# Optimization experiments

Hardware: AMD Instinct MI355X
Metric: run time of the kernel (lower is better)

Reference implementation:

```python
import jax, jax.numpy as jnp
import numpy as np

B, H, S, D = 2, 16, 4096, 64
WIN = 512
HALF = WIN // 2  # stride of the sliding window


def setup_inputs() -> dict:
    key = jax.random.key(0)
    kq, kk, kv = jax.random.split(key, 3)
    Q = jax.random.normal(kq, (B, H, S, D), dtype=jnp.float32)
    K = jax.random.normal(kk, (B, H, S, D), dtype=jnp.float32)
    V = jax.random.normal(kv, (B, H, S, D), dtype=jnp.float32)
    scale = jnp.float32(1.0 / np.sqrt(D))
    return {"Q": Q, "K": K, "V": V, "scale": scale}


def _window_attn(Q, K, V, scale):
    # sigmoid attention normalized to sum 1 over keys (use_sigmoid=True path)
    scores = jnp.einsum('...qd,...kd->...qk', Q, K) * scale
    attn = jax.nn.sigmoid(scores)
    attn = attn / jnp.sum(attn, axis=-1, keepdims=True)
    return jnp.einsum('...qk,...kd->...qd', attn, V)


def reference(Q, K, V, scale):
    b, h, s, d = Q.shape
    n_full = (s - WIN) // HALF + 1
    starts = jnp.arange(n_full) * HALF
    idx = starts[:, None] + jnp.arange(WIN)
    Qw = Q[:, :, idx, :]
    Kw = K[:, :, idx, :]
    Vw = V[:, :, idx, :]
    out_w = _window_attn(Qw, Kw, Vw, scale)

    # trailing partial window of length HALF starting at n_full*HALF
    p0 = n_full * HALF
    out_p = _window_attn(Q[:, :, p0:, :], K[:, :, p0:, :], V[:, :, p0:, :], scale)  # [b,h,HALF,d]

    alpha = jnp.linspace(0.0, 1.0, HALF, dtype=Q.dtype).reshape(1, 1, HALF, 1)
    fh = out_w[:, :, :, :HALF, :]   # first halves of each full window
    sh = out_w[:, :, :, HALF:, :]   # second halves

    a5 = alpha[:, :, None]          # [1,1,1,HALF,1]
    # overlap blend: region starting at w*HALF (w>=1) mixes window w-1's 2nd half
    # with window w's 1st half
    mid = (1 - a5) * sh[:, :, :-1] + a5 * fh[:, :, 1:]     # [b,h,n_full-1,HALF,d]
    mid = mid.reshape(b, h, (n_full - 1) * HALF, d)
    tail = (1 - alpha) * sh[:, :, -1] + alpha * out_p       # [b,h,HALF,d]
    return jnp.concatenate([fh[:, :, 0], mid, tail], axis=2)
```

## Files before the change

kernel.cpp:

```cpp
#include <hip/hip_runtime.h>
#include <stdint.h>

#define NB 2
#define NH 16
#define SEQ 4096
#define DD 64
#define NM 16
#define QB 256
#define CH 256
#define VSTR 528

typedef __attribute__((ext_vector_type(8)))  __bf16 bf16x8;
typedef __attribute__((ext_vector_type(16))) float  f32x16;
typedef __attribute__((ext_vector_type(2)))  unsigned int u32x2;

static __device__ __forceinline__ f32x16 zero16() {
    f32x16 z;
#pragma unroll
    for (int i = 0; i < 16; i++) z[i] = 0.0f;
    return z;
}

__global__ void __launch_bounds__(512, 2)
swa_kernel(const float* __restrict__ Q, const float* __restrict__ K,
           const float* __restrict__ V, const float* __restrict__ scale_p,
           float* __restrict__ out)
{
    int lid = (int)blockIdx.x;
    lid = (lid & 7) * 64 + (lid >> 3);
    const int m  = lid & 15;
    const int bh = lid >> 4;

    const float scale = scale_p[0];
    const float* Qb = Q + (size_t)bh * SEQ * DD;
    const float* Kb = K + (size_t)bh * SEQ * DD;
    const float* Vb = V + (size_t)bh * SEQ * DD;
    float*       Ob = out + (size_t)bh * SEQ * DD;

    const int tid  = threadIdx.x;
    const int lane = tid & 63;
    const int w    = tid >> 6;
    const int l31  = lane & 31;
    const int h5   = lane >> 5;

    __shared__ __align__(16) unsigned char vt[64 * VSTR];

    bf16x8 qf[4];
    {
        const float* qp = Qb + (size_t)(m * QB + w * 32 + l31) * DD + 8 * h5;
#pragma unroll
        for (int s = 0; s < 4; s++) {
            float4 a = *(const float4*)(qp + 16 * s);
            float4 b = *(const float4*)(qp + 16 * s + 4);
            bf16x8 f;
            f[0] = (__bf16)a.x; f[1] = (__bf16)a.y; f[2] = (__bf16)a.z; f[3] = (__bf16)a.w;
            f[4] = (__bf16)b.x; f[5] = (__bf16)b.y; f[6] = (__bf16)b.z; f[7] = (__bf16)b.w;
            qf[s] = f;
        }
    }

    f32x16 accA0 = zero16(), accA1 = zero16();
    f32x16 accB0 = zero16(), accB1 = zero16();
    float dA = 0.0f, dB = 0.0f;

    for (int ci = 0; ci < 3; ci++) {
        const int ck = (m - 1 + ci) * CH;
        if (ck < 0 || ck >= SEQ) continue;
        const bool inA = (m > 0) && (ci <= 1);
        const bool inB = (ci >= 1);

        __syncthreads();
        {
            const int kk = (tid & 127) * 2;
            const int dg = tid >> 7;
            const float* vp0 = Vb + (size_t)(ck + kk) * DD + dg * 16;
            const float* vp1 = vp0 + DD;
#pragma unroll
            for (int j = 0; j < 16; j += 4) {
                float4 a = *(const float4*)(vp0 + j);
                float4 b = *(const float4*)(vp1 + j);
                float av[4] = {a.x, a.y, a.z, a.w};
                float bv[4] = {b.x, b.y, b.z, b.w};
#pragma unroll
                for (int e = 0; e < 4; e++) {
                    union { __bf16 h[2]; uint32_t u; } pk;
                    pk.h[0] = (__bf16)av[e];
                    pk.h[1] = (__bf16)bv[e];
                    *(uint32_t*)(vt + (size_t)(dg * 16 + j + e) * VSTR + kk * 2) = pk.u;
                }
            }
        }
        __syncthreads();

        for (int kt = 0; kt < 8; kt++) {
            const float* kp = Kb + (size_t)(ck + kt * 32 + l31) * DD + 8 * h5;
            f32x16 st = zero16();
#pragma unroll
            for (int s = 0; s < 4; s++) {
                float4 a = *(const float4*)(kp + 16 * s);
                float4 b = *(const float4*)(kp + 16 * s + 4);
                bf16x8 f;
                f[0] = (__bf16)a.x; f[1] = (__bf16)a.y; f[2] = (__bf16)a.z; f[3] = (__bf16)a.w;
                f[4] = (__bf16)b.x; f[5] = (__bf16)b.y; f[6] = (__bf16)b.z; f[7] = (__bf16)b.w;
                st = __builtin_amdgcn_mfma_f32_32x32x16_bf16(f, qf[s], st, 0, 0, 0);
            }

            uint32_t wv[8];
            float dsum = 0.0f;
#pragma unroll
            for (int i = 0; i < 8; i++) {
                float e0 = __expf(-st[2 * i] * scale);
                float e1 = __expf(-st[2 * i + 1] * scale);
                float p0 = __builtin_amdgcn_rcpf(1.0f + e0);
                float p1 = __builtin_amdgcn_rcpf(1.0f + e1);
                union { __bf16 h[2]; uint32_t u; } pk;
                pk.h[0] = (__bf16)p0;
                pk.h[1] = (__bf16)p1;
                wv[i] = pk.u;
                dsum += (float)pk.h[0] + (float)pk.h[1];
            }
            if (inA) dA += dsum;
            if (inB) dB += dsum;

            u32x2 rA = __builtin_amdgcn_permlane32_swap(wv[0], wv[2], false, false);
            u32x2 rB = __builtin_amdgcn_permlane32_swap(wv[1], wv[3], false, false);
            u32x2 rC = __builtin_amdgcn_permlane32_swap(wv[4], wv[6], false, false);
            u32x2 rD = __builtin_amdgcn_permlane32_swap(wv[5], wv[7], false, false);
            union { uint32_t u[4]; bf16x8 v; } A0, A1;
            A0.u[0] = rA[0]; A0.u[1] = rB[0]; A0.u[2] = rA[1]; A0.u[3] = rB[1];
            A1.u[0] = rC[0]; A1.u[1] = rD[0]; A1.u[2] = rC[1]; A1.u[3] = rD[1];

            const unsigned char* vrow0 = vt + (size_t)l31 * VSTR;
            const unsigned char* vrow1 = vt + (size_t)(32 + l31) * VSTR;
            const int ko = kt * 64 + h5 * 16;
            bf16x8 v00 = *(const bf16x8*)(vrow0 + ko);
            bf16x8 v01 = *(const bf16x8*)(vrow0 + ko + 32);
            bf16x8 v10 = *(const bf16x8*)(vrow1 + ko);
            bf16x8 v11 = *(const bf16x8*)(vrow1 + ko + 32);

            if (inA) {
                accA0 = __builtin_amdgcn_mfma_f32_32x32x16_bf16(A0.v, v00, accA0, 0, 0, 0);
                accA0 = __builtin_amdgcn_mfma_f32_32x32x16_bf16(A1.v, v01, accA0, 0, 0, 0);
                accA1 = __builtin_amdgcn_mfma_f32_32x32x16_bf16(A0.v, v10, accA1, 0, 0, 0);
                accA1 = __builtin_amdgcn_mfma_f32_32x32x16_bf16(A1.v, v11, accA1, 0, 0, 0);
            }
            if (inB) {
                accB0 = __builtin_amdgcn_mfma_f32_32x32x16_bf16(A0.v, v00, accB0, 0, 0, 0);
                accB0 = __builtin_amdgcn_mfma_f32_32x32x16_bf16(A1.v, v01, accB0, 0, 0, 0);
                accB1 = __builtin_amdgcn_mfma_f32_32x32x16_bf16(A0.v, v10, accB1, 0, 0, 0);
                accB1 = __builtin_amdgcn_mfma_f32_32x32x16_bf16(A1.v, v11, accB1, 0, 0, 0);
            }
        }
    }

    const float dAt = dA + __shfl_xor(dA, 32, 64);
    const float dBt = dB + __shfl_xor(dB, 32, 64);
    const float invA = __builtin_amdgcn_rcpf(dAt);
    const float invB = __builtin_amdgcn_rcpf(dBt);

#pragma unroll
    for (int r = 0; r < 16; r++) {
        const int cr = (r & 3) + 8 * (r >> 2) + 4 * h5;
        const int j  = w * 32 + cr;
        const float ia = __shfl(invA, cr, 64);
        const float ib = __shfl(invB, cr, 64);
        float o0, o1;
        if (m == 0) {
            o0 = accB0[r] * ib;
            o1 = accB1[r] * ib;
        } else {
            const float alpha = (float)j * (1.0f / 255.0f);
            const float a0 = accA0[r] * ia, b0 = accB0[r] * ib;
            const float a1 = accA1[r] * ia, b1 = accB1[r] * ib;
            o0 = (1.0f - alpha) * a0 + alpha * b0;
            o1 = (1.0f - alpha) * a1 + alpha * b1;
        }
        float* orow = Ob + (size_t)(m * QB + j) * DD;
        orow[l31]      = o0;
        orow[32 + l31] = o1;
    }
}

extern "C" void kernel_launch(void* const* d_in, const int* in_sizes, int n_in,
                              void* d_out, int out_size, void* d_ws, size_t ws_size,
                              hipStream_t stream) {
    const float* Q = (const float*)d_in[0];
    const float* K = (const float*)d_in[1];
    const float* V = (const float*)d_in[2];
    const float* s = (const float*)d_in[3];
    float* out = (float*)d_out;
    dim3 grid(NB * NH * NM, 1, 1);
    dim3 block(512, 1, 1);
    hipLaunchKernelGGL(swa_kernel, grid, block, 0, stream, Q, K, V, s, out);
}
```

Measured before the change: 226.2 us.

## Stage K in LDS as bf16, XOR-swizzle V layout, fold scale into Q

K chunks are now loaded cooperatively once per 256-key chunk, converted to bf16 and stored in LDS in MFMA-fragment order. Each wave reads its K operands from LDS instead of re-reading fp32 K from global memory and converting it per tile. The V transpose buffer drops its padded stride for an XOR-swizzled layout to avoid bank conflicts. The scale is folded into Q before the bf16 conversion, which removes a multiply per score, and the denominator now sums fp32 sigmoids instead of the bf16-rounded values. The launch-bounds occupancy hint is raised from 2 to 4, but LDS use doubles to 64 KB per block, which may limit how many blocks fit on a CU.

```diff
diff --git a/kernel.cpp b/kernel.cpp
--- a/kernel.cpp
+++ b/kernel.cpp
@@ -8,7 +8,6 @@
 #define NM 16
 #define QB 256
 #define CH 256
-#define VSTR 528
 
 typedef __attribute__((ext_vector_type(8)))  __bf16 bf16x8;
 typedef __attribute__((ext_vector_type(16))) float  f32x16;
@@ -21,7 +20,7 @@
     return z;
 }
 
-__global__ void __launch_bounds__(512, 2)
+__global__ void __launch_bounds__(512, 4)
 swa_kernel(const float* __restrict__ Q, const float* __restrict__ K,
            const float* __restrict__ V, const float* __restrict__ scale_p,
            float* __restrict__ out)
@@ -43,7 +42,8 @@
     const int l31  = lane & 31;
     const int h5   = lane >> 5;
 
-    __shared__ __align__(16) unsigned char vt[64 * VSTR];
+    __shared__ __align__(16) unsigned char kl[32768];
+    __shared__ __align__(16) unsigned char vl[32768];
 
     bf16x8 qf[4];
     {
@@ -53,8 +53,10 @@
             float4 a = *(const float4*)(qp + 16 * s);
             float4 b = *(const float4*)(qp + 16 * s + 4);
             bf16x8 f;
-            f[0] = (__bf16)a.x; f[1] = (__bf16)a.y; f[2] = (__bf16)a.z; f[3] = (__bf16)a.w;
-            f[4] = (__bf16)b.x; f[5] = (__bf16)b.y; f[6] = (__bf16)b.z; f[7] = (__bf16)b.w;
+            f[0] = (__bf16)(a.x * scale); f[1] = (__bf16)(a.y * scale);
+            f[2] = (__bf16)(a.z * scale); f[3] = (__bf16)(a.w * scale);
+            f[4] = (__bf16)(b.x * scale); f[5] = (__bf16)(b.y * scale);
+            f[6] = (__bf16)(b.z * scale); f[7] = (__bf16)(b.w * scale);
             qf[s] = f;
         }
     }
@@ -71,6 +73,25 @@
 
         __syncthreads();
         {
+            const int key = tid >> 1, half = tid & 1;
+            const float* kp = Kb + (size_t)(ck + key) * DD + 32 * half;
+            float fl[32];
+#pragma unroll
+            for (int i = 0; i < 8; i++) {
+                float4 t = *(const float4*)(kp + 4 * i);
+                fl[4 * i] = t.x; fl[4 * i + 1] = t.y; fl[4 * i + 2] = t.z; fl[4 * i + 3] = t.w;
+            }
+#pragma unroll
+            for (int g = 0; g < 4; g++) {
+                const int sp = g >> 1, hg = g & 1;
+                const int s = 2 * half + sp;
+                bf16x8 o;
+#pragma unroll
+                for (int e = 0; e < 8; e++) o[e] = (__bf16)fl[16 * sp + 8 * hg + e];
+                *(bf16x8*)(kl + ((key >> 5) * 4 + s) * 1024 + ((key & 31) + 32 * hg) * 16) = o;
+            }
+        }
+        {
             const int kk = (tid & 127) * 2;
             const int dg = tid >> 7;
             const float* vp0 = Vb + (size_t)(ck + kk) * DD + dg * 16;
@@ -86,38 +107,33 @@
                     union { __bf16 h[2]; uint32_t u; } pk;
                     pk.h[0] = (__bf16)av[e];
                     pk.h[1] = (__bf16)bv[e];
-                    *(uint32_t*)(vt + (size_t)(dg * 16 + j + e) * VSTR + kk * 2) = pk.u;
+                    const int row = dg * 16 + j + e;
+                    *(uint32_t*)(vl + ((row * 512 + kk * 2) ^ ((row & 15) << 4))) = pk.u;
                 }
             }
         }
         __syncthreads();
 
         for (int kt = 0; kt < 8; kt++) {
-            const float* kp = Kb + (size_t)(ck + kt * 32 + l31) * DD + 8 * h5;
+            const unsigned char* kfb = kl + kt * 4096 + lane * 16;
             f32x16 st = zero16();
 #pragma unroll
             for (int s = 0; s < 4; s++) {
-                float4 a = *(const float4*)(kp + 16 * s);
-                float4 b = *(const float4*)(kp + 16 * s + 4);
-                bf16x8 f;
-                f[0] = (__bf16)a.x; f[1] = (__bf16)a.y; f[2] = (__bf16)a.z; f[3] = (__bf16)a.w;
-                f[4] = (__bf16)b.x; f[5] = (__bf16)b.y; f[6] = (__bf16)b.z; f[7] = (__bf16)b.w;
-                st = __builtin_amdgcn_mfma_f32_32x32x16_bf16(f, qf[s], st, 0, 0, 0);
+                bf16x8 kf = *(const bf16x8*)(kfb + s * 1024);
+                st = __builtin_amdgcn_mfma_f32_32x32x16_bf16(kf, qf[s], st, 0, 0, 0);
             }
 
             uint32_t wv[8];
             float dsum = 0.0f;
 #pragma unroll
             for (int i = 0; i < 8; i++) {
-                float e0 = __expf(-st[2 * i] * scale);
-                float e1 = __expf(-st[2 * i + 1] * scale);
-                float p0 = __builtin_amdgcn_rcpf(1.0f + e0);
-                float p1 = __builtin_amdgcn_rcpf(1.0f + e1);
+                float p0 = __builtin_amdgcn_rcpf(1.0f + __expf(-st[2 * i]));
+                float p1 = __builtin_amdgcn_rcpf(1.0f + __expf(-st[2 * i + 1]));
+                dsum += p0 + p1;
                 union { __bf16 h[2]; uint32_t u; } pk;
                 pk.h[0] = (__bf16)p0;
                 pk.h[1] = (__bf16)p1;
                 wv[i] = pk.u;
-                dsum += (float)pk.h[0] + (float)pk.h[1];
             }
             if (inA) dA += dsum;
             if (inB) dB += dsum;
@@ -130,13 +146,12 @@
             A0.u[0] = rA[0]; A0.u[1] = rB[0]; A0.u[2] = rA[1]; A0.u[3] = rB[1];
             A1.u[0] = rC[0]; A1.u[1] = rD[0]; A1.u[2] = rC[1]; A1.u[3] = rD[1];
 
-            const unsigned char* vrow0 = vt + (size_t)l31 * VSTR;
-            const unsigned char* vrow1 = vt + (size_t)(32 + l31) * VSTR;
             const int ko = kt * 64 + h5 * 16;
-            bf16x8 v00 = *(const bf16x8*)(vrow0 + ko);
-            bf16x8 v01 = *(const bf16x8*)(vrow0 + ko + 32);
-            bf16x8 v10 = *(const bf16x8*)(vrow1 + ko);
-            bf16x8 v11 = *(const bf16x8*)(vrow1 + ko + 32);
+            const int x0 = (l31 & 15) << 4;
+            bf16x8 v00 = *(const bf16x8*)(vl + ((l31 * 512 + ko) ^ x0));
+            bf16x8 v01 = *(const bf16x8*)(vl + ((l31 * 512 + ko + 32) ^ x0));
+            bf16x8 v10 = *(const bf16x8*)(vl + (((32 + l31) * 512 + ko) ^ x0));
+            bf16x8 v11 = *(const bf16x8*)(vl + (((32 + l31) * 512 + ko + 32) ^ x0));
 
             if (inA) {
                 accA0 = __builtin_amdgcn_mfma_f32_32x32x16_bf16(A0.v, v00, accA0, 0, 0, 0);
```

Result: slower. 389.2 us (+72.1%).

## Pre-convert K to bf16 in a workspace pass and prefetch K tiles

Applied to the files above, without the earlier changes.

Adds a separate pass that converts K from fp32 to bf16 into the workspace. The attention kernel then reads the bf16 K with register double-buffered prefetch of the next tile, which halves K read traffic and removes the conversion that was repeated inside the inner loop. The scale is also folded into Q when it is loaded, and the denominator is summed from fp32 probabilities instead of rounded ones. This costs an extra kernel launch plus a full K read and write, and the fast path only runs if the workspace is large enough.

```diff
diff --git a/kernel.cpp b/kernel.cpp
--- a/kernel.cpp
+++ b/kernel.cpp
@@ -21,10 +21,29 @@
     return z;
 }
 
+__global__ void __launch_bounds__(256)
+cvt_k_kernel(const float* __restrict__ K, __bf16* __restrict__ kw)
+{
+    const size_t gid = (size_t)blockIdx.x * 256 + threadIdx.x;
+    const float* src = K + gid * 16;
+    float4 a = *(const float4*)(src);
+    float4 b = *(const float4*)(src + 4);
+    float4 c = *(const float4*)(src + 8);
+    float4 d = *(const float4*)(src + 12);
+    bf16x8 o0, o1;
+    o0[0] = (__bf16)a.x; o0[1] = (__bf16)a.y; o0[2] = (__bf16)a.z; o0[3] = (__bf16)a.w;
+    o0[4] = (__bf16)b.x; o0[5] = (__bf16)b.y; o0[6] = (__bf16)b.z; o0[7] = (__bf16)b.w;
+    o1[0] = (__bf16)c.x; o1[1] = (__bf16)c.y; o1[2] = (__bf16)c.z; o1[3] = (__bf16)c.w;
+    o1[4] = (__bf16)d.x; o1[5] = (__bf16)d.y; o1[6] = (__bf16)d.z; o1[7] = (__bf16)d.w;
+    *(bf16x8*)(kw + gid * 16)     = o0;
+    *(bf16x8*)(kw + gid * 16 + 8) = o1;
+}
+
+template<bool PRE>
 __global__ void __launch_bounds__(512, 2)
 swa_kernel(const float* __restrict__ Q, const float* __restrict__ K,
            const float* __restrict__ V, const float* __restrict__ scale_p,
-           float* __restrict__ out)
+           const __bf16* __restrict__ kw, float* __restrict__ out)
 {
     int lid = (int)blockIdx.x;
     lid = (lid & 7) * 64 + (lid >> 3);
@@ -35,6 +54,7 @@
     const float* Qb = Q + (size_t)bh * SEQ * DD;
     const float* Kb = K + (size_t)bh * SEQ * DD;
     const float* Vb = V + (size_t)bh * SEQ * DD;
+    const __bf16* kwb = kw + (size_t)bh * SEQ * DD;
     float*       Ob = out + (size_t)bh * SEQ * DD;
 
     const int tid  = threadIdx.x;
@@ -53,8 +73,10 @@
             float4 a = *(const float4*)(qp + 16 * s);
             float4 b = *(const float4*)(qp + 16 * s + 4);
             bf16x8 f;
-            f[0] = (__bf16)a.x; f[1] = (__bf16)a.y; f[2] = (__bf16)a.z; f[3] = (__bf16)a.w;
-            f[4] = (__bf16)b.x; f[5] = (__bf16)b.y; f[6] = (__bf16)b.z; f[7] = (__bf16)b.w;
+            f[0] = (__bf16)(a.x * scale); f[1] = (__bf16)(a.y * scale);
+            f[2] = (__bf16)(a.z * scale); f[3] = (__bf16)(a.w * scale);
+            f[4] = (__bf16)(b.x * scale); f[5] = (__bf16)(b.y * scale);
+            f[6] = (__bf16)(b.z * scale); f[7] = (__bf16)(b.w * scale);
             qf[s] = f;
         }
     }
@@ -90,34 +112,52 @@
                 }
             }
         }
+
+        bf16x8 kcur[4];
+        if (PRE) {
+            const __bf16* p = kwb + (size_t)(ck + l31) * DD + 8 * h5;
+#pragma unroll
+            for (int s = 0; s < 4; s++) kcur[s] = *(const bf16x8*)(p + 16 * s);
+        }
         __syncthreads();
 
+#pragma unroll 2
         for (int kt = 0; kt < 8; kt++) {
-            const float* kp = Kb + (size_t)(ck + kt * 32 + l31) * DD + 8 * h5;
             f32x16 st = zero16();
-#pragma unroll
-            for (int s = 0; s < 4; s++) {
-                float4 a = *(const float4*)(kp + 16 * s);
-                float4 b = *(const float4*)(kp + 16 * s + 4);
-                bf16x8 f;
-                f[0] = (__bf16)a.x; f[1] = (__bf16)a.y; f[2] = (__bf16)a.z; f[3] = (__bf16)a.w;
-                f[4] = (__bf16)b.x; f[5] = (__bf16)b.y; f[6] = (__bf16)b.z; f[7] = (__bf16)b.w;
-                st = __builtin_amdgcn_mfma_f32_32x32x16_bf16(f, qf[s], st, 0, 0, 0);
+            bf16x8 knx[4];
+            if (PRE) {
+                if (kt < 7) {
+                    const __bf16* p = kwb + (size_t)(ck + (kt + 1) * 32 + l31) * DD + 8 * h5;
+#pragma unroll
+                    for (int s = 0; s < 4; s++) knx[s] = *(const bf16x8*)(p + 16 * s);
+                }
+#pragma unroll
+                for (int s = 0; s < 4; s++)
+                    st = __builtin_amdgcn_mfma_f32_32x32x16_bf16(kcur[s], qf[s], st, 0, 0, 0);
+            } else {
+                const float* kp = Kb + (size_t)(ck + kt * 32 + l31) * DD + 8 * h5;
+#pragma unroll
+                for (int s = 0; s < 4; s++) {
+                    float4 a = *(const float4*)(kp + 16 * s);
+                    float4 b = *(const float4*)(kp + 16 * s + 4);
+                    bf16x8 f;
+                    f[0] = (__bf16)a.x; f[1] = (__bf16)a.y; f[2] = (__bf16)a.z; f[3] = (__bf16)a.w;
+                    f[4] = (__bf16)b.x; f[5] = (__bf16)b.y; f[6] = (__bf16)b.z; f[7] = (__bf16)b.w;
+                    st = __builtin_amdgcn_mfma_f32_32x32x16_bf16(f, qf[s], st, 0, 0, 0);
+                }
             }
 
             uint32_t wv[8];
             float dsum = 0.0f;
 #pragma unroll
             for (int i = 0; i < 8; i++) {
-                float e0 = __expf(-st[2 * i] * scale);
-                float e1 = __expf(-st[2 * i + 1] * scale);
-                float p0 = __builtin_amdgcn_rcpf(1.0f + e0);
-                float p1 = __builtin_amdgcn_rcpf(1.0f + e1);
+                float p0 = __builtin_amdgcn_rcpf(1.0f + __expf(-st[2 * i]));
+                float p1 = __builtin_amdgcn_rcpf(1.0f + __expf(-st[2 * i + 1]));
+                dsum += p0 + p1;
                 union { __bf16 h[2]; uint32_t u; } pk;
                 pk.h[0] = (__bf16)p0;
                 pk.h[1] = (__bf16)p1;
                 wv[i] = pk.u;
-                dsum += (float)pk.h[0] + (float)pk.h[1];
             }
             if (inA) dA += dsum;
             if (inB) dB += dsum;
@@ -149,6 +189,10 @@
                 accB0 = __builtin_amdgcn_mfma_f32_32x32x16_bf16(A1.v, v01, accB0, 0, 0, 0);
                 accB1 = __builtin_amdgcn_mfma_f32_32x32x16_bf16(A0.v, v10, accB1, 0, 0, 0);
                 accB1 = __builtin_amdgcn_mfma_f32_32x32x16_bf16(A1.v, v11, accB1, 0, 0, 0);
+            }
+            if (PRE) {
+#pragma unroll
+                for (int s = 0; s < 4; s++) kcur[s] = knx[s];
             }
         }
     }
@@ -170,10 +214,8 @@
             o1 = accB1[r] * ib;
         } else {
             const float alpha = (float)j * (1.0f / 255.0f);
-            const float a0 = accA0[r] * ia, b0 = accB0[r] * ib;
-            const float a1 = accA1[r] * ia, b1 = accB1[r] * ib;
-            o0 = (1.0f - alpha) * a0 + alpha * b0;
-            o1 = (1.0f - alpha) * a1 + alpha * b1;
+            o0 = (1.0f - alpha) * (accA0[r] * ia) + alpha * (accB0[r] * ib);
+            o1 = (1.0f - alpha) * (accA1[r] * ia) + alpha * (accB1[r] * ib);
         }
         float* orow = Ob + (size_t)(m * QB + j) * DD;
         orow[l31]      = o0;
@@ -189,7 +231,19 @@
     const float* V = (const float*)d_in[2];
     const float* s = (const float*)d_in[3];
     float* out = (float*)d_out;
+
+    const size_t kElems  = (size_t)NB * NH * SEQ * DD;
+    const size_t kBytes  = kElems * sizeof(__bf16);
     dim3 grid(NB * NH * NM, 1, 1);
     dim3 block(512, 1, 1);
-    hipLaunchKernelGGL(swa_kernel, grid, block, 0, stream, Q, K, V, s, out);
-}
+
+    if (ws_size >= kBytes) {
+        __bf16* kw = (__bf16*)d_ws;
+        dim3 cg((unsigned)(kElems / 16 / 256), 1, 1);
+        hipLaunchKernelGGL(cvt_k_kernel, cg, dim3(256, 1, 1), 0, stream, K, kw);
+        hipLaunchKernelGGL((swa_kernel<true>), grid, block, 0, stream, Q, K, V, s, kw, out);
+    } else {
+        hipLaunchKernelGGL((swa_kernel<false>), grid, block, 0, stream, Q, K, V, s,
+                           (const __bf16*)nullptr, out);
+    }
+}
```

After: 193.5 us. 14.5% less time.
